# Performance work log

Hardware: AMD Instinct MI355X
Metric: run time of the kernel (lower is better)

The kernel has to match this reference:

```python
import jax, jax.numpy as jnp
import numpy as np


def setup_inputs() -> dict:
    key = jax.random.key(0)
    k1, k2 = jax.random.split(key)
    B, C, H, W = 4, 256, 64, 64
    kernel_size, ratio = 5, 2
    x = jax.random.normal(k1, (B, C, H, W), dtype=jnp.float32)
    kernel = jax.random.uniform(k2, (B, kernel_size ** 2, H * ratio, W * ratio), dtype=jnp.float32)
    return {"x": x, "kernel": kernel, "kernel_size": kernel_size, "ratio": ratio}


def reference(x, kernel, kernel_size, ratio):
    # x: [B, C, H, W]; kernel: [B, k^2, H*ratio, W*ratio]
    B, C, H, W = x.shape
    pad = kernel_size // 2  # original hardcodes padding=2 for k=5
    xp = jnp.pad(x, ((0, 0), (0, 0), (pad, pad), (pad, pad)))
    # unfold: patches[b, ki*k+kj, c, h, w] = xp[b, c, h+ki, w+kj]
    patches = jnp.stack(
        [xp[:, :, i:i + H, j:j + W] for i in range(kernel_size) for j in range(kernel_size)],
        axis=1,
    )  # [B, k2, C, H, W]
    k2 = kernel_size ** 2
    # out[b,c,h*r+p,w*r+q] = sum_k patches[b,k,c,h,w] * kernel[b,k,h*r+p,w*r+q]
    kr = kernel.reshape(B, k2, H, ratio, W, ratio)
    out = jnp.einsum('bkchw,bkhpwq->bchpwq', patches, kr)
    return out.reshape(B, C, H * ratio, W * ratio)
```

## Files before the change

kernel.cpp:

```cpp
#include <hip/hip_runtime.h>


typedef float v2 __attribute__((ext_vector_type(2)));
typedef float v4 __attribute__((ext_vector_type(4)));

__global__ __launch_bounds__(256, 4)
void carafe_kernel(const float* __restrict__ x,
                   const float* __restrict__ kern,
                   float* __restrict__ out) {
    __shared__ __align__(16) float wt[25 * 256];

    const int raw = blockIdx.x;
    const int l   = (raw & 7) * 256 + (raw >> 3);
    const int cc  = l & 7;
    const int h   = (l >> 3) & 63;
    const int b   = l >> 9;
    const int tid = threadIdx.x;
    const int t   = tid & 31;
    const int g   = tid >> 5;
    const int c0  = cc * 32 + g * 4;

    const float* kbase = kern + (size_t)b * 25 * 16384 + (size_t)(2 * h) * 128;
#pragma unroll
    for (int i = 0; i < 25; ++i)
        wt[i * 256 + tid] = kbase[(size_t)i * 16384 + tid];
    __syncthreads();

    float acc[4][2][2][2] = {};
    const float* xb = x + (size_t)(b * 256 + c0) * 4096;

#pragma unroll
    for (int ki = 0; ki < 5; ++ki) {
        const int gr = h + ki - 2;
        if ((unsigned)gr >= 64u) continue;

        float xw[4][6];
#pragma unroll
        for (int ch = 0; ch < 4; ++ch) {
            const float* rowp = xb + (size_t)ch * 4096 + gr * 64;
            const v2 A = *(const v2*)(rowp + (t ? 2 * t - 2 : 0));
            const v2 B = *(const v2*)(rowp + 2 * t);
            const v2 C = *(const v2*)(rowp + (t < 31 ? 2 * t + 2 : 60));
            xw[ch][0] = t ? A.x : 0.0f;
            xw[ch][1] = t ? A.y : 0.0f;
            xw[ch][2] = B.x;  xw[ch][3] = B.y;
            xw[ch][4] = (t < 31) ? C.x : 0.0f;
            xw[ch][5] = (t < 31) ? C.y : 0.0f;
        }

#pragma unroll
        for (int kj = 0; kj < 5; ++kj) {
            const int k = ki * 5 + kj;
            const v4 w0 = *(const v4*)&wt[k * 256 + 4 * t];
            const v4 w1 = *(const v4*)&wt[k * 256 + 128 + 4 * t];
#pragma unroll
            for (int ch = 0; ch < 4; ++ch) {
#pragma unroll
                for (int cj = 0; cj < 2; ++cj) {
                    const float xv = xw[ch][cj + kj];
                    acc[ch][cj][0][0] += w0[2 * cj]     * xv;
                    acc[ch][cj][0][1] += w0[2 * cj + 1] * xv;
                    acc[ch][cj][1][0] += w1[2 * cj]     * xv;
                    acc[ch][cj][1][1] += w1[2 * cj + 1] * xv;
                }
            }
        }
    }

#pragma unroll
    for (int ch = 0; ch < 4; ++ch) {
        float* ob = out + ((size_t)(b * 256 + c0 + ch) * 128 + 2 * h) * 128 + 4 * t;
#pragma unroll
        for (int p = 0; p < 2; ++p) {
            v4 s;
            s.x = acc[ch][0][p][0]; s.y = acc[ch][0][p][1];
            s.z = acc[ch][1][p][0]; s.w = acc[ch][1][p][1];
            *(v4*)(ob + p * 128) = s;
        }
    }
}

extern "C" void kernel_launch(void* const* d_in, const int* in_sizes, int n_in,
                              void* d_out, int out_size, void* d_ws, size_t ws_size,
                              hipStream_t stream) {
    const float* x    = (const float*)d_in[0];
    const float* kern = (const float*)d_in[1];
    float* out        = (float*)d_out;
    carafe_kernel<<<dim3(2048), dim3(256), 0, stream>>>(x, kern, out);
}
```

Measured before the change: 29.27 us.

## Double-buffer x row loads across kernel rows and vectorize weight staging

Restructures the tap loop into a software pipeline: the next input row is prefetched into a second register buffer while the current row's taps are computed, and the first row load is issued before the barrier. Row indices are clamped so loads are always issued, with the tap computation guarded instead. Weight staging into shared memory now uses 16-byte vector loads in a strided loop. Launch bounds minimum blocks drop from 4 to 3 to give room for the extra registers, at the cost of lower occupancy.

```diff
diff --git a/kernel.cpp b/kernel.cpp
--- a/kernel.cpp
+++ b/kernel.cpp
@@ -4,7 +4,46 @@
 typedef float v2 __attribute__((ext_vector_type(2)));
 typedef float v4 __attribute__((ext_vector_type(4)));
 
-__global__ __launch_bounds__(256, 4)
+#define LOADROW(BUF, KI)                                                       \
+    {                                                                          \
+        int gr_ = h + (KI) - 2;                                                \
+        gr_ = gr_ < 0 ? 0 : (gr_ > 63 ? 63 : gr_);                             \
+        _Pragma("unroll")                                                      \
+        for (int ch = 0; ch < 4; ++ch) {                                       \
+            const float* rowp = xb + (size_t)ch * 4096 + gr_ * 64;             \
+            const v2 A = *(const v2*)(rowp + (t ? 2 * t - 2 : 0));             \
+            const v2 B = *(const v2*)(rowp + 2 * t);                           \
+            const v2 C = *(const v2*)(rowp + (t < 31 ? 2 * t + 2 : 60));       \
+            BUF[ch][0] = t ? A.x : 0.0f;                                       \
+            BUF[ch][1] = t ? A.y : 0.0f;                                       \
+            BUF[ch][2] = B.x;  BUF[ch][3] = B.y;                               \
+            BUF[ch][4] = (t < 31) ? C.x : 0.0f;                                \
+            BUF[ch][5] = (t < 31) ? C.y : 0.0f;                                \
+        }                                                                      \
+    }
+
+#define TAPS(BUF, KI)                                                          \
+    if ((unsigned)(h + (KI) - 2) < 64u) {                                      \
+        _Pragma("unroll")                                                      \
+        for (int kj = 0; kj < 5; ++kj) {                                       \
+            const int k = (KI) * 5 + kj;                                       \
+            const v4 w0 = *(const v4*)&wt[k * 256 + 4 * t];                    \
+            const v4 w1 = *(const v4*)&wt[k * 256 + 128 + 4 * t];              \
+            _Pragma("unroll")                                                  \
+            for (int ch = 0; ch < 4; ++ch) {                                   \
+                _Pragma("unroll")                                              \
+                for (int cj = 0; cj < 2; ++cj) {                               \
+                    const float xv = BUF[ch][cj + kj];                         \
+                    acc[ch][cj][0][0] += w0[2 * cj]     * xv;                  \
+                    acc[ch][cj][0][1] += w0[2 * cj + 1] * xv;                  \
+                    acc[ch][cj][1][0] += w1[2 * cj]     * xv;                  \
+                    acc[ch][cj][1][1] += w1[2 * cj + 1] * xv;                  \
+                }                                                              \
+            }                                                                  \
+        }                                                                      \
+    }
+
+__global__ __launch_bounds__(256, 3)
 void carafe_kernel(const float* __restrict__ x,
                    const float* __restrict__ kern,
                    float* __restrict__ out) {
@@ -20,52 +59,29 @@
     const int g   = tid >> 5;
     const int c0  = cc * 32 + g * 4;
 
-    const float* kbase = kern + (size_t)b * 25 * 16384 + (size_t)(2 * h) * 128;
-#pragma unroll
-    for (int i = 0; i < 25; ++i)
-        wt[i * 256 + tid] = kbase[(size_t)i * 16384 + tid];
+    const float* xb = x + (size_t)(b * 256 + c0) * 4096;
+
+    {
+        const float* kbase = kern + (size_t)b * 25 * 16384 + (size_t)(2 * h) * 128;
+        for (int idx = tid; idx < 1600; idx += 256) {
+            const int f = idx * 4;
+            const int k = f >> 8;
+            const int r = f & 255;
+            *(v4*)&wt[f] = *(const v4*)(kbase + (size_t)k * 16384 + r);
+        }
+    }
+
+    float acc[4][2][2][2] = {};
+    float xwa[4][6], xwb[4][6];
+
+    LOADROW(xwa, 0);
     __syncthreads();
 
-    float acc[4][2][2][2] = {};
-    const float* xb = x + (size_t)(b * 256 + c0) * 4096;
-
-#pragma unroll
-    for (int ki = 0; ki < 5; ++ki) {
-        const int gr = h + ki - 2;
-        if ((unsigned)gr >= 64u) continue;
-
-        float xw[4][6];
-#pragma unroll
-        for (int ch = 0; ch < 4; ++ch) {
-            const float* rowp = xb + (size_t)ch * 4096 + gr * 64;
-            const v2 A = *(const v2*)(rowp + (t ? 2 * t - 2 : 0));
-            const v2 B = *(const v2*)(rowp + 2 * t);
-            const v2 C = *(const v2*)(rowp + (t < 31 ? 2 * t + 2 : 60));
-            xw[ch][0] = t ? A.x : 0.0f;
-            xw[ch][1] = t ? A.y : 0.0f;
-            xw[ch][2] = B.x;  xw[ch][3] = B.y;
-            xw[ch][4] = (t < 31) ? C.x : 0.0f;
-            xw[ch][5] = (t < 31) ? C.y : 0.0f;
-        }
-
-#pragma unroll
-        for (int kj = 0; kj < 5; ++kj) {
-            const int k = ki * 5 + kj;
-            const v4 w0 = *(const v4*)&wt[k * 256 + 4 * t];
-            const v4 w1 = *(const v4*)&wt[k * 256 + 128 + 4 * t];
-#pragma unroll
-            for (int ch = 0; ch < 4; ++ch) {
-#pragma unroll
-                for (int cj = 0; cj < 2; ++cj) {
-                    const float xv = xw[ch][cj + kj];
-                    acc[ch][cj][0][0] += w0[2 * cj]     * xv;
-                    acc[ch][cj][0][1] += w0[2 * cj + 1] * xv;
-                    acc[ch][cj][1][0] += w1[2 * cj]     * xv;
-                    acc[ch][cj][1][1] += w1[2 * cj + 1] * xv;
-                }
-            }
-        }
-    }
+    LOADROW(xwb, 1);  TAPS(xwa, 0);
+    LOADROW(xwa, 2);  TAPS(xwb, 1);
+    LOADROW(xwb, 3);  TAPS(xwa, 2);
+    LOADROW(xwa, 4);  TAPS(xwb, 3);
+                      TAPS(xwa, 4);
 
 #pragma unroll
     for (int ch = 0; ch < 4; ++ch) {
```

Result: slower. 30.42 us (+3.9%).
